# Optimization experiments

Measured on AMD Instinct MI355X. Metric: run time of the kernel, lower is better.

## Reference

```python
import jax, jax.numpy as jnp
import numpy as np

# Model/config dims (Llama-3-8B style attention, GQA 32q/8kv)
B, S, HID = 4, 512, 4096
NH, NKV, D = 32, 8, 128
CAP = 2048          # KV cache capacity
MAXPOS = 2048       # max_position_embeddings
START = 1024        # kvcache_start_index (uniform across batch -> static masking)
EPS = 1e-6
QK_SCALE = 1.0 / float(D) ** 0.5
NEG = -1e9


def setup_inputs() -> dict:
    key = jax.random.key(0)
    ks = jax.random.split(key, 8)
    w = 0.02  # weight init scale
    return {
        'hidden_states': jax.random.normal(ks[0], (B, S, HID), jnp.float32),
        'k_cache': jax.random.normal(ks[1], (B, NKV, CAP, D), jnp.float32),
        'v_cache': jax.random.normal(ks[2], (B, NKV, CAP, D), jnp.float32),
        'rope_rotary_cos_sin': jax.random.uniform(ks[3], (B, MAXPOS, D), jnp.float32),
        'context_lengths': jnp.full((B,), S, jnp.int32),
        'kvcache_start_index': jnp.full((B,), START, jnp.int32),
        'Wq': jax.random.normal(ks[4], (HID, NH * D), jnp.float32) * w,
        'Wk': jax.random.normal(ks[5], (HID, NKV * D), jnp.float32) * w,
        'Wv': jax.random.normal(ks[6], (HID, NKV * D), jnp.float32) * w,
        'Wo': jax.random.normal(ks[7], (NH * D, HID), jnp.float32) * w,
        'q_norm_w': jnp.ones((D,), jnp.float32),
        'k_norm_w': jnp.ones((D,), jnp.float32),
    }


def _rmsnorm(x, w):
    # per-head RMSNorm over head_dim (Qwen3-style QK norm)
    return x * jax.lax.rsqrt(jnp.mean(x * x, axis=-1, keepdims=True) + EPS) * w


def _apply_rope(x, cos, sin, pos):
    # x: [B,H,S,D]; cos/sin: [MAXPOS, D/2]; pos: [B,S]
    c = cos[pos][:, None, :, :]  # [B,1,S,D/2]
    s = sin[pos][:, None, :, :]
    x1, x2 = jnp.split(x, 2, axis=-1)
    return jnp.concatenate([x1 * c - x2 * s, x2 * c + x1 * s], axis=-1)


def reference(hidden_states, k_cache, v_cache, rope_rotary_cos_sin,
              context_lengths, kvcache_start_index,
              Wq, Wk, Wv, Wo, q_norm_w, k_norm_w):
    b, s, _ = hidden_states.shape
    # fused QKV projection
    q = (hidden_states @ Wq).reshape(b, s, NH, D)
    k = (hidden_states @ Wk).reshape(b, s, NKV, D)
    v = (hidden_states @ Wv).reshape(b, s, NKV, D)
    # QK norm
    q = _rmsnorm(q, q_norm_w)
    k = _rmsnorm(k, k_norm_w)
    # [B,H,S,D]
    q = q.transpose(0, 2, 1, 3)
    k = k.transpose(0, 2, 1, 3)
    v = v.transpose(0, 2, 1, 3)
    # RoPE tables: first half cos, second half sin; batch dim 0 only
    half = D // 2
    cos = rope_rotary_cos_sin[0, :, :half]
    sin = rope_rotary_cos_sin[0, :, half:]
    pos = kvcache_start_index[:, None] + jnp.arange(s, dtype=kvcache_start_index.dtype)[None, :]
    q = _apply_rope(q, cos, sin, pos)
    k = _apply_rope(k, cos, sin, pos)
    # KV cache update: write new k/v at per-batch start index
    def upd(cache, new, st):  # cache [H,CAP,D], new [H,S,D]
        return jax.lax.dynamic_update_slice(cache, new, (0, st, 0))
    present_k = jax.vmap(upd)(k_cache, k, kvcache_start_index)
    present_v = jax.vmap(upd)(v_cache, v, kvcache_start_index)
    # GQA: expand kv heads to attention heads
    g = NH // NKV
    kf = jnp.repeat(present_k, g, axis=1)  # [B,NH,CAP,D]
    vf = jnp.repeat(present_v, g, axis=1)
    # scaled attention over cache; mask cols beyond absolute query position
    scores = jnp.einsum('bhsd,bhtd->bhst', q * QK_SCALE, kf)
    col = jnp.arange(CAP, dtype=pos.dtype)
    allowed = col[None, None, :] <= pos[:, :, None]        # [B,S,CAP]
    scores = jnp.where(allowed[:, None, :, :], scores, NEG)
    attn = jax.nn.softmax(scores, axis=-1)
    out = jnp.einsum('bhst,bhtd->bhsd', attn, vf)
    out = out.transpose(0, 2, 1, 3).reshape(b, s, NH * D)
    out = out @ Wo
    return out, present_k, present_v
```

## Files before the change

### kernel.cpp

```cpp
#include <hip/hip_runtime.h>
#include <hip/hip_bf16.h>
#include <cstdint>

#define Bsz   4
#define Ssz   512
#define HIDsz 4096
#define NHsz  32
#define NKVsz 8
#define Dsz   128
#define CAPsz 2048
#define EPSf  1e-6f
#define QK_SCALEf 0.08838834764831845f

typedef __attribute__((ext_vector_type(8))) short short8;
typedef __attribute__((ext_vector_type(4))) float f32x4;

__device__ __forceinline__ unsigned short f2bf(float x) {
    unsigned u = __float_as_uint(x);
    return (unsigned short)((u + 0x7fffu + ((u >> 16) & 1u)) >> 16);
}

__device__ __forceinline__ void gload16(const void* g, void* l) {
    __builtin_amdgcn_global_load_lds(
        (const __attribute__((address_space(1))) unsigned int*)g,
        (__attribute__((address_space(3))) unsigned int*)l, 16, 0, 0);
}

__global__ __launch_bounds__(256) void convert_bf16_kernel(
    const float* __restrict__ in, unsigned short* __restrict__ out, int n4)
{
    int i = blockIdx.x * blockDim.x + threadIdx.x;
    if (i < n4) {
        float4 v = ((const float4*)in)[i];
        ushort4 o;
        o.x = f2bf(v.x); o.y = f2bf(v.y); o.z = f2bf(v.z); o.w = f2bf(v.w);
        ((ushort4*)out)[i] = o;
    }
}

__global__ __launch_bounds__(256) void transpose_bf16_kernel(
    const float* __restrict__ W, unsigned short* __restrict__ Wt, int K, int N)
{
    __shared__ float tile[64][65];
    const int k0 = blockIdx.y * 64, n0 = blockIdx.x * 64;
    const int t = threadIdx.x;
    const int tr = t >> 4, tc4 = (t & 15) * 4;
#pragma unroll
    for (int i = 0; i < 4; i++) {
        int r = tr + i * 16;
        float4 v = *(const float4*)(W + (size_t)(k0 + r) * N + n0 + tc4);
        tile[r][tc4 + 0] = v.x; tile[r][tc4 + 1] = v.y;
        tile[r][tc4 + 2] = v.z; tile[r][tc4 + 3] = v.w;
    }
    __syncthreads();
#pragma unroll
    for (int i = 0; i < 4; i++) {
        int nr = tr + i * 16;
        ushort4 o;
        o.x = f2bf(tile[tc4 + 0][nr]);
        o.y = f2bf(tile[tc4 + 1][nr]);
        o.z = f2bf(tile[tc4 + 2][nr]);
        o.w = f2bf(tile[tc4 + 3][nr]);
        *(ushort4*)(Wt + (size_t)(n0 + nr) * K + k0 + tc4) = o;
    }
}

__global__ __launch_bounds__(256) void transpose_v_kernel(
    const float* __restrict__ V, unsigned short* __restrict__ Vt)
{
    __shared__ float tile[64][65];
    const int c0 = blockIdx.x * 64, d0 = blockIdx.y * 64, bk = blockIdx.z;
    const int t = threadIdx.x;
    const int tr = t >> 4, tc4 = (t & 15) * 4;
    const float* base = V + (size_t)bk * CAPsz * Dsz;
#pragma unroll
    for (int i = 0; i < 4; i++) {
        int r = tr + i * 16;
        float4 v = *(const float4*)(base + (size_t)(c0 + r) * Dsz + d0 + tc4);
        tile[r][tc4 + 0] = v.x; tile[r][tc4 + 1] = v.y;
        tile[r][tc4 + 2] = v.z; tile[r][tc4 + 3] = v.w;
    }
    __syncthreads();
    unsigned short* ob = Vt + (size_t)bk * Dsz * CAPsz;
#pragma unroll
    for (int i = 0; i < 4; i++) {
        int dr = tr + i * 16;
        ushort4 o;
        o.x = f2bf(tile[tc4 + 0][dr]);
        o.y = f2bf(tile[tc4 + 1][dr]);
        o.z = f2bf(tile[tc4 + 2][dr]);
        o.w = f2bf(tile[tc4 + 3][dr]);
        *(ushort4*)(ob + (size_t)(d0 + dr) * CAPsz + c0 + tc4) = o;
    }
}

__global__ __launch_bounds__(256, 2) void gemm_bf16_kernel(
    const unsigned short* __restrict__ A,
    const unsigned short* __restrict__ Bt,
    float* __restrict__ C, int M, int N, int K)
{
    __shared__ __align__(16) unsigned short As[128 * 64];
    __shared__ __align__(16) unsigned short Bs[128 * 64];
    const int t    = threadIdx.x;
    const int lane = t & 63, wv = t >> 6;
    const int m0 = blockIdx.y * 128, n0 = blockIdx.x * 128;
    const int rw = (wv & 1) * 64, cw = (wv >> 1) * 64;

    f32x4 acc[4][4];
#pragma unroll
    for (int r = 0; r < 4; r++)
#pragma unroll
        for (int c = 0; c < 4; c++) acc[r][c] = (f32x4){0.f, 0.f, 0.f, 0.f};

    const int arow = lane >> 3;
    const int acol = (lane & 7) * 8;
    const int fr = lane & 15, fq = (lane >> 4) * 8;

    for (int k0 = 0; k0 < K; k0 += 64) {
        __syncthreads();
#pragma unroll
        for (int i = 0; i < 4; i++) {
            int ro = (i * 4 + wv) * 8;
            gload16(A  + (size_t)(m0 + ro + arow) * K + k0 + acol, As + (size_t)ro * 64);
            gload16(Bt + (size_t)(n0 + ro + arow) * K + k0 + acol, Bs + (size_t)ro * 64);
        }
        __syncthreads();
#pragma unroll
        for (int kk = 0; kk < 2; kk++) {
            short8 af[4], bfr[4];
#pragma unroll
            for (int r = 0; r < 4; r++)
                af[r] = *(const short8*)&As[(rw + r * 16 + fr) * 64 + kk * 32 + fq];
#pragma unroll
            for (int c = 0; c < 4; c++)
                bfr[c] = *(const short8*)&Bs[(cw + c * 16 + fr) * 64 + kk * 32 + fq];
#pragma unroll
            for (int r = 0; r < 4; r++)
#pragma unroll
                for (int c = 0; c < 4; c++)
                    acc[r][c] = __builtin_amdgcn_mfma_f32_16x16x32_bf16(
                        af[r], bfr[c], acc[r][c], 0, 0, 0);
        }
    }

#pragma unroll
    for (int r = 0; r < 4; r++) {
#pragma unroll
        for (int c = 0; c < 4; c++) {
            int col = n0 + cw + c * 16 + (lane & 15);
#pragma unroll
            for (int reg = 0; reg < 4; reg++) {
                int row = m0 + rw + r * 16 + (lane >> 4) * 4 + reg;
                C[(size_t)row * N + col] = acc[r][c][reg];
            }
        }
    }
}

__global__ __launch_bounds__(256, 2) void gemm_qkv_kernel(
    const unsigned short* __restrict__ A,
    const unsigned short* __restrict__ Bt,
    float* __restrict__ Cq,
    float* __restrict__ Ck,
    float* __restrict__ Cv,
    const int* __restrict__ start_idx)
{
    __shared__ __align__(16) unsigned short As[128 * 64];
    __shared__ __align__(16) unsigned short Bs[128 * 64];
    const int t    = threadIdx.x;
    const int lane = t & 63, wv = t >> 6;
    const int m0 = blockIdx.y * 128, n0 = blockIdx.x * 128;
    const int rw = (wv & 1) * 64, cw = (wv >> 1) * 64;

    f32x4 acc[4][4];
#pragma unroll
    for (int r = 0; r < 4; r++)
#pragma unroll
        for (int c = 0; c < 4; c++) acc[r][c] = (f32x4){0.f, 0.f, 0.f, 0.f};

    const int arow = lane >> 3;
    const int acol = (lane & 7) * 8;
    const int fr = lane & 15, fq = (lane >> 4) * 8;

    for (int k0 = 0; k0 < HIDsz; k0 += 64) {
        __syncthreads();
#pragma unroll
        for (int i = 0; i < 4; i++) {
            int ro = (i * 4 + wv) * 8;
            gload16(A  + (size_t)(m0 + ro + arow) * HIDsz + k0 + acol, As + (size_t)ro * 64);
            gload16(Bt + (size_t)(n0 + ro + arow) * HIDsz + k0 + acol, Bs + (size_t)ro * 64);
        }
        __syncthreads();
#pragma unroll
        for (int kk = 0; kk < 2; kk++) {
            short8 af[4], bfr[4];
#pragma unroll
            for (int r = 0; r < 4; r++)
                af[r] = *(const short8*)&As[(rw + r * 16 + fr) * 64 + kk * 32 + fq];
#pragma unroll
            for (int c = 0; c < 4; c++)
                bfr[c] = *(const short8*)&Bs[(cw + c * 16 + fr) * 64 + kk * 32 + fq];
#pragma unroll
            for (int r = 0; r < 4; r++)
#pragma unroll
                for (int c = 0; c < 4; c++)
                    acc[r][c] = __builtin_amdgcn_mfma_f32_16x16x32_bf16(
                        af[r], bfr[c], acc[r][c], 0, 0, 0);
        }
    }

    const int pos0 = start_idx[m0 >> 9];
    const bool isQ = (n0 < 4096);
    const bool isK = (n0 >= 4096) && (n0 < 5120);
    float* dst = isK ? Ck : Cv;
    const int cbase = isK ? 4096 : 5120;
#pragma unroll
    for (int r = 0; r < 4; r++) {
#pragma unroll
        for (int c = 0; c < 4; c++) {
            int col = n0 + cw + c * 16 + (lane & 15);
#pragma unroll
            for (int reg = 0; reg < 4; reg++) {
                int row = m0 + rw + r * 16 + (lane >> 4) * 4 + reg;
                float val = acc[r][c][reg];
                if (isQ) {
                    Cq[(size_t)row * 4096 + col] = val;
                } else {
                    int cc = col - cbase;
                    int pos = pos0 + (row & (Ssz - 1));
                    int b = row >> 9;
                    dst[((size_t)(b * NKVsz + (cc >> 7)) * CAPsz + pos) * Dsz + (cc & 127)] = val;
                }
            }
        }
    }
}

__global__ __launch_bounds__(256) void rmsnorm_rope_kernel(
    float* __restrict__ X, unsigned short* __restrict__ Xbf,
    const float* __restrict__ w,
    const float* __restrict__ rope, const int* __restrict__ start_idx,
    int nheads, int mode)
{
    int gid   = blockIdx.x * blockDim.x + threadIdx.x;
    int wid   = gid >> 6;
    int lane  = threadIdx.x & 63;
    int token = wid / nheads;
    int h     = wid - token * nheads;
    int b = token >> 9, s = token & (Ssz - 1);
    int pos = start_idx[b] + s;
    float* row;
    if (mode == 0) row = X + (size_t)token * (nheads * Dsz) + h * Dsz;
    else           row = X + ((size_t)(b * nheads + h) * CAPsz + pos) * Dsz;

    float x1 = row[lane], x2 = row[lane + 64];
    float ss = x1 * x1 + x2 * x2;
#pragma unroll
    for (int off = 32; off > 0; off >>= 1) ss += __shfl_xor(ss, off);
    float rn  = rsqrtf(ss * (1.f / 128.f) + EPSf);
    float xn1 = x1 * rn * w[lane];
    float xn2 = x2 * rn * w[lane + 64];
    float c   = rope[(size_t)pos * Dsz + lane];
    float sn  = rope[(size_t)pos * Dsz + 64 + lane];
    float o1 = xn1 * c - xn2 * sn;
    float o2 = xn2 * c + xn1 * sn;
    if (mode == 0) {
        unsigned short* orow = Xbf + (size_t)token * (nheads * Dsz) + h * Dsz;
        orow[lane]      = f2bf(o1 * QK_SCALEf);
        orow[lane + 64] = f2bf(o2 * QK_SCALEf);
    } else {
        row[lane]      = o1;
        row[lane + 64] = o2;
    }
}

__global__ __launch_bounds__(256, 2) void attn_mfma_kernel(
    const unsigned short* __restrict__ Qbf,
    const unsigned short* __restrict__ Kbf,
    const unsigned short* __restrict__ Vtbf,
    unsigned short* __restrict__ O,
    const int* __restrict__ start_idx)
{
    __shared__ __align__(16) unsigned short Ks[64 * 128];
    __shared__ __align__(16) unsigned short Vs[128 * 64];
    __shared__ __align__(16) unsigned short Ps[4][32 * 72];

    const int t = threadIdx.x, lane = t & 63, wv = t >> 6;
    const int l15 = lane & 15, l4 = lane >> 4;
    const int qt = blockIdx.x, kv = blockIdx.y, b = blockIdx.z;
    const int h = kv * 4 + wv;
    const int s0 = qt * 32;
    const int start = start_idx[b];

    const int swz = (l15 & 7) << 3;

    short8 aq[2][4];
    const unsigned short* qb = Qbf + ((size_t)(b * Ssz + s0)) * HIDsz + h * Dsz;
#pragma unroll
    for (int m2 = 0; m2 < 2; m2++)
#pragma unroll
        for (int kq = 0; kq < 4; kq++)
            aq[m2][kq] = *(const short8*)(qb + (size_t)(m2 * 16 + l15) * HIDsz + kq * 32 + l4 * 8);

    f32x4 Oacc[2][8];
    float m_run[2][4], l_run[2][4];
#pragma unroll
    for (int m2 = 0; m2 < 2; m2++) {
#pragma unroll
        for (int nd = 0; nd < 8; nd++) Oacc[m2][nd] = (f32x4){0.f, 0.f, 0.f, 0.f};
#pragma unroll
        for (int r = 0; r < 4; r++) { m_run[m2][r] = -1e30f; l_run[m2][r] = 0.f; }
    }

    const unsigned short* kb = Kbf + (size_t)(b * NKVsz + kv) * CAPsz * Dsz;
    const unsigned short* vb = Vtbf + (size_t)(b * NKVsz + kv) * (size_t)Dsz * CAPsz;

    int t_hi = start + s0 + 31;
    if (t_hi > CAPsz - 1) t_hi = CAPsz - 1;

    int krow[4], vrow[4];
    unsigned short* kw[4];
    unsigned short* vw[4];
#pragma unroll
    for (int i = 0; i < 4; i++) {
        int kr = (i * 4 + wv) * 4 + l4;
        krow[i] = kr;
        kw[i] = &Ks[kr * 128 + ((l15 * 8) ^ ((kr & 7) << 3))];
        int vr = (i * 4 + wv) * 8 + (lane >> 3);
        vrow[i] = vr;
        vw[i] = &Vs[vr * 64 + (((lane & 7) * 8) ^ ((vr & 7) << 3))];
    }

    short8 kreg[4], vreg[4];
#pragma unroll
    for (int i = 0; i < 4; i++) {
        kreg[i] = *(const short8*)(kb + (size_t)krow[i] * Dsz + l15 * 8);
        vreg[i] = *(const short8*)(vb + (size_t)vrow[i] * CAPsz + (lane & 7) * 8);
    }

    for (int t0 = 0; t0 <= t_hi; t0 += 64) {
        asm volatile("s_waitcnt lgkmcnt(0)" ::: "memory");
        __builtin_amdgcn_s_barrier();
        __builtin_amdgcn_sched_barrier(0);

#pragma unroll
        for (int i = 0; i < 4; i++) *(short8*)kw[i] = kreg[i];
#pragma unroll
        for (int i = 0; i < 4; i++) *(short8*)vw[i] = vreg[i];

        if (t0 + 64 <= t_hi) {
            int tn = t0 + 64;
#pragma unroll
            for (int i = 0; i < 4; i++) {
                kreg[i] = *(const short8*)(kb + (size_t)(tn + krow[i]) * Dsz + l15 * 8);
                vreg[i] = *(const short8*)(vb + (size_t)vrow[i] * CAPsz + tn + (lane & 7) * 8);
            }
        }

        asm volatile("s_waitcnt lgkmcnt(0)" ::: "memory");
        __builtin_amdgcn_s_barrier();
        __builtin_amdgcn_sched_barrier(0);

        f32x4 Sacc[2][4];
#pragma unroll
        for (int m2 = 0; m2 < 2; m2++)
#pragma unroll
            for (int n = 0; n < 4; n++) Sacc[m2][n] = (f32x4){0.f, 0.f, 0.f, 0.f};
        __builtin_amdgcn_s_setprio(1);
#pragma unroll
        for (int kq = 0; kq < 4; kq++) {
            short8 bk[4];
#pragma unroll
            for (int n = 0; n < 4; n++)
                bk[n] = *(const short8*)&Ks[(n * 16 + l15) * 128 + ((kq * 32 + l4 * 8) ^ swz)];
#pragma unroll
            for (int m2 = 0; m2 < 2; m2++)
#pragma unroll
                for (int n = 0; n < 4; n++)
                    Sacc[m2][n] = __builtin_amdgcn_mfma_f32_16x16x32_bf16(
                        aq[m2][kq], bk[n], Sacc[m2][n], 0, 0, 0);
        }
        __builtin_amdgcn_s_setprio(0);

        bool need_mask = (t0 + 63) > (start + s0);
#pragma unroll
        for (int m2 = 0; m2 < 2; m2++) {
#pragma unroll
            for (int reg = 0; reg < 4; reg++) {
                int rloc = m2 * 16 + l4 * 4 + reg;
                int row_pos = start + s0 + rloc;
                float sv[4];
#pragma unroll
                for (int n = 0; n < 4; n++) {
                    sv[n] = Sacc[m2][n][reg];
                    if (need_mask && (t0 + n * 16 + l15 > row_pos)) sv[n] = -1e30f;
                }
                float mrow = fmaxf(fmaxf(sv[0], sv[1]), fmaxf(sv[2], sv[3]));
#pragma unroll
                for (int off = 1; off < 16; off <<= 1)
                    mrow = fmaxf(mrow, __shfl_xor(mrow, off));
                float m_new = fmaxf(m_run[m2][reg], mrow);
                float alpha = __expf(m_run[m2][reg] - m_new);
                float ps = 0.f;
#pragma unroll
                for (int n = 0; n < 4; n++) {
                    sv[n] = __expf(sv[n] - m_new);
                    ps += sv[n];
                }
#pragma unroll
                for (int off = 1; off < 16; off <<= 1)
                    ps += __shfl_xor(ps, off);
                l_run[m2][reg] = l_run[m2][reg] * alpha + ps;
                m_run[m2][reg] = m_new;
#pragma unroll
                for (int nd = 0; nd < 8; nd++) Oacc[m2][nd][reg] *= alpha;
#pragma unroll
                for (int n = 0; n < 4; n++)
                    Ps[wv][rloc * 72 + n * 16 + l15] = f2bf(sv[n]);
            }
        }

        __builtin_amdgcn_s_setprio(1);
#pragma unroll
        for (int kp = 0; kp < 2; kp++) {
            short8 ap[2];
#pragma unroll
            for (int m2 = 0; m2 < 2; m2++)
                ap[m2] = *(const short8*)&Ps[wv][(m2 * 16 + l15) * 72 + kp * 32 + l4 * 8];
#pragma unroll
            for (int nd = 0; nd < 8; nd++) {
                short8 bv = *(const short8*)&Vs[(nd * 16 + l15) * 64 + ((kp * 32 + l4 * 8) ^ swz)];
#pragma unroll
                for (int m2 = 0; m2 < 2; m2++)
                    Oacc[m2][nd] = __builtin_amdgcn_mfma_f32_16x16x32_bf16(
                        ap[m2], bv, Oacc[m2][nd], 0, 0, 0);
            }
        }
        __builtin_amdgcn_s_setprio(0);
    }

    unsigned short* ob = O + ((size_t)(b * Ssz + s0)) * HIDsz + h * Dsz;
#pragma unroll
    for (int m2 = 0; m2 < 2; m2++)
#pragma unroll
        for (int reg = 0; reg < 4; reg++) {
            int rloc = m2 * 16 + l4 * 4 + reg;
            float inv = 1.f / l_run[m2][reg];
#pragma unroll
            for (int nd = 0; nd < 8; nd++)
                ob[(size_t)rloc * HIDsz + nd * 16 + l15] = f2bf(Oacc[m2][nd][reg] * inv);
        }
}

extern "C" void kernel_launch(void* const* d_in, const int* in_sizes, int n_in,
                              void* d_out, int out_size, void* d_ws, size_t ws_size,
                              hipStream_t stream) {
    (void)in_sizes; (void)n_in; (void)out_size; (void)ws_size;
    const float* hidden    = (const float*)d_in[0];
    const float* k_cache   = (const float*)d_in[1];
    const float* v_cache   = (const float*)d_in[2];
    const float* rope      = (const float*)d_in[3];
    const int*   start_idx = (const int*)d_in[5];
    const float* Wq        = (const float*)d_in[6];
    const float* Wk        = (const float*)d_in[7];
    const float* Wv        = (const float*)d_in[8];
    const float* Wo        = (const float*)d_in[9];
    const float* q_norm_w  = (const float*)d_in[10];
    const float* k_norm_w  = (const float*)d_in[11];

    float* out   = (float*)d_out;
    float* out_k = out + (size_t)Bsz * Ssz * HIDsz;
    float* out_v = out_k + (size_t)Bsz * NKVsz * CAPsz * Dsz;

    char* ws = (char*)d_ws;
    float*          q_ws      = (float*)ws;
    unsigned short* Kbf       = (unsigned short*)ws;
    unsigned short* Vtbf      = (unsigned short*)(ws + (((size_t) 16) << 20));
    unsigned short* hidden_bf = (unsigned short*)(ws + (((size_t) 32) << 20));
    unsigned short* attn_bf   = (unsigned short*)(ws + (((size_t) 48) << 20));
    unsigned short* qbf       = (unsigned short*)(ws + (((size_t) 64) << 20));
    unsigned short* Wqkv_t    = (unsigned short*)(ws + (((size_t) 80) << 20));
    unsigned short* Wk_t      = Wqkv_t + (size_t)4096 * 4096;
    unsigned short* Wv_t      = Wqkv_t + (size_t)5120 * 4096;
    unsigned short* Wo_t      = Wqkv_t;

    const size_t cache_bytes = (size_t)Bsz * NKVsz * CAPsz * Dsz * sizeof(float);
    (void)hipMemcpyAsync(out_k, k_cache, cache_bytes, hipMemcpyDeviceToDevice, stream);
    (void)hipMemcpyAsync(out_v, v_cache, cache_bytes, hipMemcpyDeviceToDevice, stream);

    convert_bf16_kernel<<<8192, 256, 0, stream>>>(hidden, hidden_bf, 2048 * 4096 / 4);
    transpose_bf16_kernel<<<dim3(64, 64), 256, 0, stream>>>(Wq, Wqkv_t, HIDsz, NHsz * Dsz);
    transpose_bf16_kernel<<<dim3(16, 64), 256, 0, stream>>>(Wk, Wk_t, HIDsz, NKVsz * Dsz);
    transpose_bf16_kernel<<<dim3(16, 64), 256, 0, stream>>>(Wv, Wv_t, HIDsz, NKVsz * Dsz);

    gemm_qkv_kernel<<<dim3(48, 16), 256, 0, stream>>>(
        hidden_bf, Wqkv_t, q_ws, out_k, out_v, start_idx);

    rmsnorm_rope_kernel<<<16384, 256, 0, stream>>>(q_ws, qbf, q_norm_w, rope, start_idx, NHsz, 0);
    rmsnorm_rope_kernel<<<4096, 256, 0, stream>>>(out_k, nullptr, k_norm_w, rope, start_idx, NKVsz, 1);

    convert_bf16_kernel<<<8192, 256, 0, stream>>>(out_k, Kbf, Bsz * NKVsz * CAPsz * Dsz / 4);
    transpose_v_kernel<<<dim3(32, 2, 32), 256, 0, stream>>>(out_v, Vtbf);

    attn_mfma_kernel<<<dim3(16, NKVsz, Bsz), 256, 0, stream>>>(qbf, Kbf, Vtbf, attn_bf, start_idx);

    transpose_bf16_kernel<<<dim3(64, 64), 256, 0, stream>>>(Wo, Wo_t, NHsz * Dsz, HIDsz);
    gemm_bf16_kernel<<<dim3(32, 16), 256, 0, stream>>>(attn_bf, Wo_t, out, 2048, 4096, 4096);
}
```

Before: 673.3 us.

## Skip unused cache conversion, merge weight transposes, halve attention query tile

The RMSNorm/RoPE kernel for K now writes the bf16 copy directly, and the full-cache K conversion is replaced by one that converts only the prefix before the start index. The V transpose skips tiles beyond the causal range. The three QKV weight transposes are merged into a single launch. Attention moves to 16-query tiles with twice as many blocks, and occupancy hints on the GEMMs and attention are raised to 3 blocks per CU, which may cause register spills.

```diff
diff --git a/kernel.cpp b/kernel.cpp
--- a/kernel.cpp
+++ b/kernel.cpp
@@ -38,6 +38,20 @@
     }
 }
 
+__global__ __launch_bounds__(256) void convert_k_prefix_kernel(
+    const float* __restrict__ in, unsigned short* __restrict__ out,
+    const int* __restrict__ start_idx)
+{
+    int i = blockIdx.x * blockDim.x + threadIdx.x;
+    int pos = (i >> 5) & (CAPsz - 1);
+    int b   = i >> 19;
+    if (pos >= start_idx[b]) return;
+    float4 v = ((const float4*)in)[i];
+    ushort4 o;
+    o.x = f2bf(v.x); o.y = f2bf(v.y); o.z = f2bf(v.z); o.w = f2bf(v.w);
+    ((ushort4*)out)[i] = o;
+}
+
 __global__ __launch_bounds__(256) void transpose_bf16_kernel(
     const float* __restrict__ W, unsigned short* __restrict__ Wt, int K, int N)
 {
@@ -65,11 +79,47 @@
     }
 }
 
+__global__ __launch_bounds__(256) void transpose_wqkv_kernel(
+    const float* __restrict__ Wq, const float* __restrict__ Wk,
+    const float* __restrict__ Wv, unsigned short* __restrict__ Wt)
+{
+    __shared__ float tile[64][65];
+    const int nt = blockIdx.x;
+    const int k0 = blockIdx.y * 64;
+    const float* W; int srcN, c0;
+    if (nt < 64)      { W = Wq; srcN = 4096; c0 = nt * 64; }
+    else if (nt < 80) { W = Wk; srcN = 1024; c0 = (nt - 64) * 64; }
+    else              { W = Wv; srcN = 1024; c0 = (nt - 80) * 64; }
+    const int t = threadIdx.x;
+    const int tr = t >> 4, tc4 = (t & 15) * 4;
+#pragma unroll
+    for (int i = 0; i < 4; i++) {
+        int r = tr + i * 16;
+        float4 v = *(const float4*)(W + (size_t)(k0 + r) * srcN + c0 + tc4);
+        tile[r][tc4 + 0] = v.x; tile[r][tc4 + 1] = v.y;
+        tile[r][tc4 + 2] = v.z; tile[r][tc4 + 3] = v.w;
+    }
+    __syncthreads();
+    const int n0 = nt * 64;
+#pragma unroll
+    for (int i = 0; i < 4; i++) {
+        int nr = tr + i * 16;
+        ushort4 o;
+        o.x = f2bf(tile[tc4 + 0][nr]);
+        o.y = f2bf(tile[tc4 + 1][nr]);
+        o.z = f2bf(tile[tc4 + 2][nr]);
+        o.w = f2bf(tile[tc4 + 3][nr]);
+        *(ushort4*)(Wt + (size_t)(n0 + nr) * HIDsz + k0 + tc4) = o;
+    }
+}
+
 __global__ __launch_bounds__(256) void transpose_v_kernel(
-    const float* __restrict__ V, unsigned short* __restrict__ Vt)
+    const float* __restrict__ V, unsigned short* __restrict__ Vt,
+    const int* __restrict__ start_idx)
 {
     __shared__ float tile[64][65];
     const int c0 = blockIdx.x * 64, d0 = blockIdx.y * 64, bk = blockIdx.z;
+    if (c0 >= start_idx[bk >> 3] + Ssz) return;
     const int t = threadIdx.x;
     const int tr = t >> 4, tc4 = (t & 15) * 4;
     const float* base = V + (size_t)bk * CAPsz * Dsz;
@@ -94,7 +144,7 @@
     }
 }
 
-__global__ __launch_bounds__(256, 2) void gemm_bf16_kernel(
+__global__ __launch_bounds__(256, 3) void gemm_bf16_kernel(
     const unsigned short* __restrict__ A,
     const unsigned short* __restrict__ Bt,
     float* __restrict__ C, int M, int N, int K)
@@ -157,7 +207,7 @@
     }
 }
 
-__global__ __launch_bounds__(256, 2) void gemm_qkv_kernel(
+__global__ __launch_bounds__(256, 3) void gemm_qkv_kernel(
     const unsigned short* __restrict__ A,
     const unsigned short* __restrict__ Bt,
     float* __restrict__ Cq,
@@ -249,14 +299,15 @@
     int h     = wid - token * nheads;
     int b = token >> 9, s = token & (Ssz - 1);
     int pos = start_idx[b] + s;
-    float* row;
-    if (mode == 0) row = X + (size_t)token * (nheads * Dsz) + h * Dsz;
-    else           row = X + ((size_t)(b * nheads + h) * CAPsz + pos) * Dsz;
+    size_t off;
+    if (mode == 0) off = (size_t)token * (nheads * Dsz) + h * Dsz;
+    else           off = ((size_t)(b * nheads + h) * CAPsz + pos) * Dsz;
+    float* row = X + off;
 
     float x1 = row[lane], x2 = row[lane + 64];
     float ss = x1 * x1 + x2 * x2;
 #pragma unroll
-    for (int off = 32; off > 0; off >>= 1) ss += __shfl_xor(ss, off);
+    for (int off2 = 32; off2 > 0; off2 >>= 1) ss += __shfl_xor(ss, off2);
     float rn  = rsqrtf(ss * (1.f / 128.f) + EPSf);
     float xn1 = x1 * rn * w[lane];
     float xn2 = x2 * rn * w[lane + 64];
@@ -265,16 +316,19 @@
     float o1 = xn1 * c - xn2 * sn;
     float o2 = xn2 * c + xn1 * sn;
     if (mode == 0) {
-        unsigned short* orow = Xbf + (size_t)token * (nheads * Dsz) + h * Dsz;
+        unsigned short* orow = Xbf + off;
         orow[lane]      = f2bf(o1 * QK_SCALEf);
         orow[lane + 64] = f2bf(o2 * QK_SCALEf);
     } else {
         row[lane]      = o1;
         row[lane + 64] = o2;
-    }
-}
-
-__global__ __launch_bounds__(256, 2) void attn_mfma_kernel(
+        unsigned short* orow = Xbf + off;
+        orow[lane]      = f2bf(o1);
+        orow[lane + 64] = f2bf(o2);
+    }
+}
+
+__global__ __launch_bounds__(256, 3) void attn_mfma_kernel(
     const unsigned short* __restrict__ Qbf,
     const unsigned short* __restrict__ Kbf,
     const unsigned short* __restrict__ Vtbf,
@@ -283,39 +337,34 @@
 {
     __shared__ __align__(16) unsigned short Ks[64 * 128];
     __shared__ __align__(16) unsigned short Vs[128 * 64];
-    __shared__ __align__(16) unsigned short Ps[4][32 * 72];
+    __shared__ __align__(16) unsigned short Ps[4][16 * 72];
 
     const int t = threadIdx.x, lane = t & 63, wv = t >> 6;
     const int l15 = lane & 15, l4 = lane >> 4;
     const int qt = blockIdx.x, kv = blockIdx.y, b = blockIdx.z;
     const int h = kv * 4 + wv;
-    const int s0 = qt * 32;
+    const int s0 = qt * 16;
     const int start = start_idx[b];
 
     const int swz = (l15 & 7) << 3;
 
-    short8 aq[2][4];
+    short8 aq[4];
     const unsigned short* qb = Qbf + ((size_t)(b * Ssz + s0)) * HIDsz + h * Dsz;
 #pragma unroll
-    for (int m2 = 0; m2 < 2; m2++)
-#pragma unroll
-        for (int kq = 0; kq < 4; kq++)
-            aq[m2][kq] = *(const short8*)(qb + (size_t)(m2 * 16 + l15) * HIDsz + kq * 32 + l4 * 8);
-
-    f32x4 Oacc[2][8];
-    float m_run[2][4], l_run[2][4];
-#pragma unroll
-    for (int m2 = 0; m2 < 2; m2++) {
-#pragma unroll
-        for (int nd = 0; nd < 8; nd++) Oacc[m2][nd] = (f32x4){0.f, 0.f, 0.f, 0.f};
-#pragma unroll
-        for (int r = 0; r < 4; r++) { m_run[m2][r] = -1e30f; l_run[m2][r] = 0.f; }
-    }
+    for (int kq = 0; kq < 4; kq++)
+        aq[kq] = *(const short8*)(qb + (size_t)l15 * HIDsz + kq * 32 + l4 * 8);
+
+    f32x4 Oacc[8];
+    float m_run[4], l_run[4];
+#pragma unroll
+    for (int nd = 0; nd < 8; nd++) Oacc[nd] = (f32x4){0.f, 0.f, 0.f, 0.f};
+#pragma unroll
+    for (int r = 0; r < 4; r++) { m_run[r] = -1e30f; l_run[r] = 0.f; }
 
     const unsigned short* kb = Kbf + (size_t)(b * NKVsz + kv) * CAPsz * Dsz;
     const unsigned short* vb = Vtbf + (size_t)(b * NKVsz + kv) * (size_t)Dsz * CAPsz;
 
-    int t_hi = start + s0 + 31;
+    int t_hi = start + s0 + 15;
     if (t_hi > CAPsz - 1) t_hi = CAPsz - 1;
 
     int krow[4], vrow[4];
@@ -361,11 +410,9 @@
         __builtin_amdgcn_s_barrier();
         __builtin_amdgcn_sched_barrier(0);
 
-        f32x4 Sacc[2][4];
-#pragma unroll
-        for (int m2 = 0; m2 < 2; m2++)
-#pragma unroll
-            for (int n = 0; n < 4; n++) Sacc[m2][n] = (f32x4){0.f, 0.f, 0.f, 0.f};
+        f32x4 Sacc[4];
+#pragma unroll
+        for (int n = 0; n < 4; n++) Sacc[n] = (f32x4){0.f, 0.f, 0.f, 0.f};
         __builtin_amdgcn_s_setprio(1);
 #pragma unroll
         for (int kq = 0; kq < 4; kq++) {
@@ -374,66 +421,56 @@
             for (int n = 0; n < 4; n++)
                 bk[n] = *(const short8*)&Ks[(n * 16 + l15) * 128 + ((kq * 32 + l4 * 8) ^ swz)];
 #pragma unroll
-            for (int m2 = 0; m2 < 2; m2++)
-#pragma unroll
-                for (int n = 0; n < 4; n++)
-                    Sacc[m2][n] = __builtin_amdgcn_mfma_f32_16x16x32_bf16(
-                        aq[m2][kq], bk[n], Sacc[m2][n], 0, 0, 0);
+            for (int n = 0; n < 4; n++)
+                Sacc[n] = __builtin_amdgcn_mfma_f32_16x16x32_bf16(
+                    aq[kq], bk[n], Sacc[n], 0, 0, 0);
         }
         __builtin_amdgcn_s_setprio(0);
 
         bool need_mask = (t0 + 63) > (start + s0);
 #pragma unroll
-        for (int m2 = 0; m2 < 2; m2++) {
-#pragma unroll
-            for (int reg = 0; reg < 4; reg++) {
-                int rloc = m2 * 16 + l4 * 4 + reg;
-                int row_pos = start + s0 + rloc;
-                float sv[4];
-#pragma unroll
-                for (int n = 0; n < 4; n++) {
-                    sv[n] = Sacc[m2][n][reg];
-                    if (need_mask && (t0 + n * 16 + l15 > row_pos)) sv[n] = -1e30f;
-                }
-                float mrow = fmaxf(fmaxf(sv[0], sv[1]), fmaxf(sv[2], sv[3]));
-#pragma unroll
-                for (int off = 1; off < 16; off <<= 1)
-                    mrow = fmaxf(mrow, __shfl_xor(mrow, off));
-                float m_new = fmaxf(m_run[m2][reg], mrow);
-                float alpha = __expf(m_run[m2][reg] - m_new);
-                float ps = 0.f;
-#pragma unroll
-                for (int n = 0; n < 4; n++) {
-                    sv[n] = __expf(sv[n] - m_new);
-                    ps += sv[n];
-                }
-#pragma unroll
-                for (int off = 1; off < 16; off <<= 1)
-                    ps += __shfl_xor(ps, off);
-                l_run[m2][reg] = l_run[m2][reg] * alpha + ps;
-                m_run[m2][reg] = m_new;
-#pragma unroll
-                for (int nd = 0; nd < 8; nd++) Oacc[m2][nd][reg] *= alpha;
-#pragma unroll
-                for (int n = 0; n < 4; n++)
-                    Ps[wv][rloc * 72 + n * 16 + l15] = f2bf(sv[n]);
+        for (int reg = 0; reg < 4; reg++) {
+            int rloc = l4 * 4 + reg;
+            int row_pos = start + s0 + rloc;
+            float sv[4];
+#pragma unroll
+            for (int n = 0; n < 4; n++) {
+                sv[n] = Sacc[n][reg];
+                if (need_mask && (t0 + n * 16 + l15 > row_pos)) sv[n] = -1e30f;
             }
+            float mrow = fmaxf(fmaxf(sv[0], sv[1]), fmaxf(sv[2], sv[3]));
+#pragma unroll
+            for (int off = 1; off < 16; off <<= 1)
+                mrow = fmaxf(mrow, __shfl_xor(mrow, off));
+            float m_new = fmaxf(m_run[reg], mrow);
+            float alpha = __expf(m_run[reg] - m_new);
+            float ps = 0.f;
+#pragma unroll
+            for (int n = 0; n < 4; n++) {
+                sv[n] = __expf(sv[n] - m_new);
+                ps += sv[n];
+            }
+#pragma unroll
+            for (int off = 1; off < 16; off <<= 1)
+                ps += __shfl_xor(ps, off);
+            l_run[reg] = l_run[reg] * alpha + ps;
+            m_run[reg] = m_new;
+#pragma unroll
+            for (int nd = 0; nd < 8; nd++) Oacc[nd][reg] *= alpha;
+#pragma unroll
+            for (int n = 0; n < 4; n++)
+                Ps[wv][rloc * 72 + n * 16 + l15] = f2bf(sv[n]);
         }
 
         __builtin_amdgcn_s_setprio(1);
 #pragma unroll
         for (int kp = 0; kp < 2; kp++) {
-            short8 ap[2];
-#pragma unroll
-            for (int m2 = 0; m2 < 2; m2++)
-                ap[m2] = *(const short8*)&Ps[wv][(m2 * 16 + l15) * 72 + kp * 32 + l4 * 8];
+            short8 ap = *(const short8*)&Ps[wv][l15 * 72 + kp * 32 + l4 * 8];
 #pragma unroll
             for (int nd = 0; nd < 8; nd++) {
                 short8 bv = *(const short8*)&Vs[(nd * 16 + l15) * 64 + ((kp * 32 + l4 * 8) ^ swz)];
-#pragma unroll
-                for (int m2 = 0; m2 < 2; m2++)
-                    Oacc[m2][nd] = __builtin_amdgcn_mfma_f32_16x16x32_bf16(
-                        ap[m2], bv, Oacc[m2][nd], 0, 0, 0);
+                Oacc[nd] = __builtin_amdgcn_mfma_f32_16x16x32_bf16(
+                    ap, bv, Oacc[nd], 0, 0, 0);
             }
         }
         __builtin_amdgcn_s_setprio(0);
@@ -441,15 +478,13 @@
 
     unsigned short* ob = O + ((size_t)(b * Ssz + s0)) * HIDsz + h * Dsz;
 #pragma unroll
-    for (int m2 = 0; m2 < 2; m2++)
-#pragma unroll
-        for (int reg = 0; reg < 4; reg++) {
-            int rloc = m2 * 16 + l4 * 4 + reg;
-            float inv = 1.f / l_run[m2][reg];
-#pragma unroll
-            for (int nd = 0; nd < 8; nd++)
-                ob[(size_t)rloc * HIDsz + nd * 16 + l15] = f2bf(Oacc[m2][nd][reg] * inv);
-        }
+    for (int reg = 0; reg < 4; reg++) {
+        int rloc = l4 * 4 + reg;
+        float inv = 1.f / l_run[reg];
+#pragma unroll
+        for (int nd = 0; nd < 8; nd++)
+            ob[(size_t)rloc * HIDsz + nd * 16 + l15] = f2bf(Oacc[nd][reg] * inv);
+    }
 }
 
 extern "C" void kernel_launch(void* const* d_in, const int* in_sizes, int n_in,
@@ -480,8 +515,6 @@
     unsigned short* attn_bf   = (unsigned short*)(ws + (((size_t) 48) << 20));
     unsigned short* qbf       = (unsigned short*)(ws + (((size_t) 64) << 20));
     unsigned short* Wqkv_t    = (unsigned short*)(ws + (((size_t) 80) << 20));
-    unsigned short* Wk_t      = Wqkv_t + (size_t)4096 * 4096;
-    unsigned short* Wv_t      = Wqkv_t + (size_t)5120 * 4096;
     unsigned short* Wo_t      = Wqkv_t;
 
     const size_t cache_bytes = (size_t)Bsz * NKVsz * CAPsz * Dsz * sizeof(float);
@@ -489,20 +522,18 @@
     (void)hipMemcpyAsync(out_v, v_cache, cache_bytes, hipMemcpyDeviceToDevice, stream);
 
     convert_bf16_kernel<<<8192, 256, 0, stream>>>(hidden, hidden_bf, 2048 * 4096 / 4);
-    transpose_bf16_kernel<<<dim3(64, 64), 256, 0, stream>>>(Wq, Wqkv_t, HIDsz, NHsz * Dsz);
-    transpose_bf16_kernel<<<dim3(16, 64), 256, 0, stream>>>(Wk, Wk_t, HIDsz, NKVsz * Dsz);
-    transpose_bf16_kernel<<<dim3(16, 64), 256, 0, stream>>>(Wv, Wv_t, HIDsz, NKVsz * Dsz);
+    transpose_wqkv_kernel<<<dim3(96, 64), 256, 0, stream>>>(Wq, Wk, Wv, Wqkv_t);
 
     gemm_qkv_kernel<<<dim3(48, 16), 256, 0, stream>>>(
         hidden_bf, Wqkv_t, q_ws, out_k, out_v, start_idx);
 
     rmsnorm_rope_kernel<<<16384, 256, 0, stream>>>(q_ws, qbf, q_norm_w, rope, start_idx, NHsz, 0);
-    rmsnorm_rope_kernel<<<4096, 256, 0, stream>>>(out_k, nullptr, k_norm_w, rope, start_idx, NKVsz, 1);
-
-    convert_bf16_kernel<<<8192, 256, 0, stream>>>(out_k, Kbf, Bsz * NKVsz * CAPsz * Dsz / 4);
-    transpose_v_kernel<<<dim3(32, 2, 32), 256, 0, stream>>>(out_v, Vtbf);
-
-    attn_mfma_kernel<<<dim3(16, NKVsz, Bsz), 256, 0, stream>>>(qbf, Kbf, Vtbf, attn_bf, start_idx);
+    rmsnorm_rope_kernel<<<4096, 256, 0, stream>>>(out_k, Kbf, k_norm_w, rope, start_idx, NKVsz, 1);
+
+    convert_k_prefix_kernel<<<8192, 256, 0, stream>>>(out_k, Kbf, start_idx);
+    transpose_v_kernel<<<dim3(32, 2, 32), 256, 0, stream>>>(out_v, Vtbf, start_idx);
+
+    attn_mfma_kernel<<<dim3(32, NKVsz, Bsz), 256, 0, stream>>>(qbf, Kbf, Vtbf, attn_bf, start_idx);
 
     transpose_bf16_kernel<<<dim3(64, 64), 256, 0, stream>>>(Wo, Wo_t, NHsz * Dsz, HIDsz);
     gemm_bf16_kernel<<<dim3(32, 16), 256, 0, stream>>>(attn_bf, Wo_t, out, 2048, 4096, 4096);
```

Result: no change. 683.4 us (+1.5%).
